# Optimization experiments

Hardware: AMD Instinct MI355X
Metric: run time of the kernel (lower is better)

The kernel has to match this reference:

```python
import jax, jax.numpy as jnp
import numpy as np


def setup_inputs() -> dict:
    key = jax.random.key(0)
    B, n = 1048576, 8
    x = jax.random.normal(key, (B, n, n), dtype=jnp.float32)
    return {"x": x, "num_iters": 5}


def reference(x, num_iters):
    # FusedMHC.forward: flatten to [B, n, n] in fp32, run Sinkhorn, cast back.
    input_dtype = x.dtype
    n = x.shape[-1]
    M = jnp.exp(x.reshape(-1, n, n).astype(jnp.float32))  # positive kernel matrix
    # num_iters alternating row / column normalizations (Sinkhorn-Knopp)
    for _ in range(num_iters):
        M = M / jnp.sum(M, axis=-1, keepdims=True)  # row normalize
        M = M / jnp.sum(M, axis=-2, keepdims=True)  # col normalize
    return M.reshape(x.shape).astype(input_dtype)
```

## Files before the change

kernel.cpp:

```cpp
#include <hip/hip_runtime.h>


#define N 8

typedef float f32x4 __attribute__((ext_vector_type(4)));

template <int CTRL>
__device__ __forceinline__ float dpp_xor(float x) {
    int r = __builtin_amdgcn_update_dpp(0, __float_as_int(x), CTRL, 0xF, 0xF, true);
    return __int_as_float(r);
}

__device__ __forceinline__ void exp8(f32x4 v0, f32x4 v1, float* r) {
    r[0] = __expf(v0.x); r[1] = __expf(v0.y);
    r[2] = __expf(v0.z); r[3] = __expf(v0.w);
    r[4] = __expf(v1.x); r[5] = __expf(v1.y);
    r[6] = __expf(v1.z); r[7] = __expf(v1.w);
}

__device__ __forceinline__ void row_norm(float* r) {
    float s = ((r[0] + r[1]) + (r[2] + r[3])) + ((r[4] + r[5]) + (r[6] + r[7]));
    float inv = __builtin_amdgcn_rcpf(s);
#pragma unroll
    for (int i = 0; i < 8; ++i) r[i] *= inv;
}

__device__ __forceinline__ void col_norm(float* r) {
#pragma unroll
    for (int i = 0; i < 8; ++i) {
        float c = r[i];
        c += dpp_xor<0xB1>(c);
        c += dpp_xor<0x4E>(c);
        c += dpp_xor<0x128>(c);
        r[i] *= __builtin_amdgcn_rcpf(c);
    }
}

__device__ __forceinline__ void store8(f32x4* __restrict__ o4, size_t idx,
                                       const float* r) {
    f32x4 v0 = {r[0], r[1], r[2], r[3]};
    f32x4 v1 = {r[4], r[5], r[6], r[7]};
    o4[idx] = v0;
    o4[idx + 1] = v1;
}

__global__ __launch_bounds__(256) void sinkhorn8_kernel(
    const float* __restrict__ x,
    float* __restrict__ out,
    const int* __restrict__ num_iters_p,
    int nwaves)
{
    int T = blockIdx.x * blockDim.x + threadIdx.x;
    int w = T >> 6;
    if (w >= nwaves) return;

    const int num_iters = *num_iters_p;

    int l = T & 63;
    int g = l >> 4;
    int t = l & 15;
    int b = (t >> 2) & 1;
    int row = (t & 3) | ((t >> 1) & 4);

    size_t base = (size_t)w * 512 + (size_t)g * 32 + (size_t)b * 16 + (size_t)row * 2;

    const f32x4* x4 = (const f32x4*)x;
    f32x4* o4 = (f32x4*)out;

    f32x4 a0 = x4[base + 0],   a1 = x4[base + 1];
    f32x4 b0 = x4[base + 128], b1 = x4[base + 129];
    f32x4 c0 = x4[base + 256], c1 = x4[base + 257];
    f32x4 d0 = x4[base + 384], d1 = x4[base + 385];

    float A[8], Bv[8], C[8], D[8];
    exp8(a0, a1, A);
    exp8(b0, b1, Bv);
    exp8(c0, c1, C);
    exp8(d0, d1, D);

    for (int it = 0; it < num_iters; ++it) {
        row_norm(A); row_norm(Bv); row_norm(C); row_norm(D);
        col_norm(A); col_norm(Bv); col_norm(C); col_norm(D);
    }

    store8(o4, base + 0, A);
    store8(o4, base + 128, Bv);
    store8(o4, base + 256, C);
    store8(o4, base + 384, D);
}

__global__ __launch_bounds__(64) void sinkhorn8_tail(
    const float* __restrict__ x,
    float* __restrict__ out,
    const int* __restrict__ num_iters_p,
    int nfull, int B)
{
    int m = nfull + blockIdx.x * blockDim.x + threadIdx.x;
    if (m >= B) return;
    const int num_iters = *num_iters_p;

    float M[N * N];
    const f32x4* xv = (const f32x4*)(x + (size_t)m * (N * N));
    f32x4* ov = (f32x4*)(out + (size_t)m * (N * N));
#pragma unroll
    for (int k = 0; k < 16; ++k) {
        f32x4 v = xv[k];
        M[4 * k + 0] = __expf(v.x);
        M[4 * k + 1] = __expf(v.y);
        M[4 * k + 2] = __expf(v.z);
        M[4 * k + 3] = __expf(v.w);
    }
    for (int it = 0; it < num_iters; ++it) {
#pragma unroll
        for (int r = 0; r < N; ++r) {
            float s = 0.f;
#pragma unroll
            for (int c = 0; c < N; ++c) s += M[r * N + c];
            float inv = __builtin_amdgcn_rcpf(s);
#pragma unroll
            for (int c = 0; c < N; ++c) M[r * N + c] *= inv;
        }
#pragma unroll
        for (int c = 0; c < N; ++c) {
            float s = 0.f;
#pragma unroll
            for (int r = 0; r < N; ++r) s += M[r * N + c];
            float inv = __builtin_amdgcn_rcpf(s);
#pragma unroll
            for (int r = 0; r < N; ++r) M[r * N + c] *= inv;
        }
    }
#pragma unroll
    for (int k = 0; k < 16; ++k) {
        f32x4 v = {M[4 * k], M[4 * k + 1], M[4 * k + 2], M[4 * k + 3]};
        ov[k] = v;
    }
}

extern "C" void kernel_launch(void* const* d_in, const int* in_sizes, int n_in,
                              void* d_out, int out_size, void* d_ws, size_t ws_size,
                              hipStream_t stream) {
    const float* x = (const float*)d_in[0];
    const int* num_iters = (const int*)d_in[1];
    float* out = (float*)d_out;

    int B = in_sizes[0] / (N * N);
    int nwaves = B / 32;
    int nfull = nwaves * 32;

    if (nwaves > 0) {
        long long threads = (long long)nwaves * 64;
        int block = 256;
        long long grid = (threads + block - 1) / block;
        sinkhorn8_kernel<<<(int)grid, block, 0, stream>>>(x, out, num_iters, nwaves);
    }
    int tail = B - nfull;
    if (tail > 0) {
        sinkhorn8_tail<<<1, 64, 0, stream>>>(x, out, num_iters, nfull, B);
    }
}
```

Before: 435.2 us.

## Split each matrix row across two lanes, halving per-thread work

Each thread now holds half a row (one float4) per matrix instead of a full row (two float4s), so a wave covers 16 matrices instead of 32 and the grid doubles. Row sums gain a cross-lane shuffle (xor 4) to combine the two halves. Column sums still use DPP butterflies, now over four columns per lane. The intent is more parallelism and fewer registers per thread, in exchange for an extra cross-lane reduction each iteration and twice as many waves to launch.

Measured after the change: 434.2 us. No clear change (-0.2%).

```diff
diff --git a/kernel.cpp b/kernel.cpp
--- a/kernel.cpp
+++ b/kernel.cpp
@@ -11,37 +11,35 @@
     return __int_as_float(r);
 }
 
-__device__ __forceinline__ void exp8(f32x4 v0, f32x4 v1, float* r) {
-    r[0] = __expf(v0.x); r[1] = __expf(v0.y);
-    r[2] = __expf(v0.z); r[3] = __expf(v0.w);
-    r[4] = __expf(v1.x); r[5] = __expf(v1.y);
-    r[6] = __expf(v1.z); r[7] = __expf(v1.w);
+__device__ __forceinline__ void exp4(f32x4& v) {
+    v.x = __expf(v.x);
+    v.y = __expf(v.y);
+    v.z = __expf(v.z);
+    v.w = __expf(v.w);
 }
 
-__device__ __forceinline__ void row_norm(float* r) {
-    float s = ((r[0] + r[1]) + (r[2] + r[3])) + ((r[4] + r[5]) + (r[6] + r[7]));
-    float inv = __builtin_amdgcn_rcpf(s);
-#pragma unroll
-    for (int i = 0; i < 8; ++i) r[i] *= inv;
+__device__ __forceinline__ void row_norm(f32x4& v) {
+    float rs = (v.x + v.y) + (v.z + v.w);
+    rs += __shfl_xor(rs, 4, 64);
+    float rinv = __builtin_amdgcn_rcpf(rs);
+    v.x *= rinv;
+    v.y *= rinv;
+    v.z *= rinv;
+    v.w *= rinv;
 }
 
-__device__ __forceinline__ void col_norm(float* r) {
-#pragma unroll
-    for (int i = 0; i < 8; ++i) {
-        float c = r[i];
-        c += dpp_xor<0xB1>(c);
-        c += dpp_xor<0x4E>(c);
-        c += dpp_xor<0x128>(c);
-        r[i] *= __builtin_amdgcn_rcpf(c);
-    }
-}
-
-__device__ __forceinline__ void store8(f32x4* __restrict__ o4, size_t idx,
-                                       const float* r) {
-    f32x4 v0 = {r[0], r[1], r[2], r[3]};
-    f32x4 v1 = {r[4], r[5], r[6], r[7]};
-    o4[idx] = v0;
-    o4[idx + 1] = v1;
+__device__ __forceinline__ void col_norm(f32x4& v) {
+    float cx = v.x, cy = v.y, cz = v.z, cw = v.w;
+    cx += dpp_xor<0xB1>(cx);  cy += dpp_xor<0xB1>(cy);
+    cz += dpp_xor<0xB1>(cz);  cw += dpp_xor<0xB1>(cw);
+    cx += dpp_xor<0x4E>(cx);  cy += dpp_xor<0x4E>(cy);
+    cz += dpp_xor<0x4E>(cz);  cw += dpp_xor<0x4E>(cw);
+    cx += dpp_xor<0x128>(cx); cy += dpp_xor<0x128>(cy);
+    cz += dpp_xor<0x128>(cz); cw += dpp_xor<0x128>(cw);
+    v.x *= __builtin_amdgcn_rcpf(cx);
+    v.y *= __builtin_amdgcn_rcpf(cy);
+    v.z *= __builtin_amdgcn_rcpf(cz);
+    v.w *= __builtin_amdgcn_rcpf(cw);
 }
 
 __global__ __launch_bounds__(256) void sinkhorn8_kernel(
@@ -59,34 +57,30 @@
     int l = T & 63;
     int g = l >> 4;
     int t = l & 15;
-    int b = (t >> 2) & 1;
+    int h = (t >> 2) & 1;
     int row = (t & 3) | ((t >> 1) & 4);
 
-    size_t base = (size_t)w * 512 + (size_t)g * 32 + (size_t)b * 16 + (size_t)row * 2;
+    size_t base = (size_t)w * 256 + (size_t)(g * 16 + row * 2 + h);
 
     const f32x4* x4 = (const f32x4*)x;
     f32x4* o4 = (f32x4*)out;
 
-    f32x4 a0 = x4[base + 0],   a1 = x4[base + 1];
-    f32x4 b0 = x4[base + 128], b1 = x4[base + 129];
-    f32x4 c0 = x4[base + 256], c1 = x4[base + 257];
-    f32x4 d0 = x4[base + 384], d1 = x4[base + 385];
+    f32x4 A = x4[base + 0];
+    f32x4 Bv = x4[base + 64];
+    f32x4 C = x4[base + 128];
+    f32x4 D = x4[base + 192];
 
-    float A[8], Bv[8], C[8], D[8];
-    exp8(a0, a1, A);
-    exp8(b0, b1, Bv);
-    exp8(c0, c1, C);
-    exp8(d0, d1, D);
+    exp4(A); exp4(Bv); exp4(C); exp4(D);
 
     for (int it = 0; it < num_iters; ++it) {
         row_norm(A); row_norm(Bv); row_norm(C); row_norm(D);
         col_norm(A); col_norm(Bv); col_norm(C); col_norm(D);
     }
 
-    store8(o4, base + 0, A);
-    store8(o4, base + 128, Bv);
-    store8(o4, base + 256, C);
-    store8(o4, base + 384, D);
+    o4[base + 0] = A;
+    o4[base + 64] = Bv;
+    o4[base + 128] = C;
+    o4[base + 192] = D;
 }
 
 __global__ __launch_bounds__(64) void sinkhorn8_tail(
@@ -145,8 +139,8 @@
     float* out = (float*)d_out;
 
     int B = in_sizes[0] / (N * N);
-    int nwaves = B / 32;
-    int nfull = nwaves * 32;
+    int nwaves = B / 16;
+    int nfull = nwaves * 16;
 
     if (nwaves > 0) {
         long long threads = (long long)nwaves * 64;
```
